# Kernel tuning notes

Hardware: AMD Instinct MI355X
Metric: run time of the kernel (lower is better)

The kernel has to match this reference:

```python
import jax, jax.numpy as jnp
import numpy as np

B, L, K = 4, 2048, 30
NS, NV = 1024, 256   # node hidden (scalar, vector)
ES, EV = 32, 1       # edge hidden (scalar, vector)
CLAMP = 32           # clamp_rel_pos
PE = 16              # num positional embeddings

def _nan_to_num(t):
    return jnp.where(jnp.isfinite(t), t, jnp.zeros((), t.dtype))

def _norm(t, axis=-1, keepdims=False, eps=1e-8):
    return jnp.sqrt(jnp.sum(t * t, axis=axis, keepdims=keepdims) + eps)

def _normalize(t, axis=-1):
    return _nan_to_num(t / _norm(t, axis=axis, keepdims=True))

def _norm_no_nan(t, axis=-1, keepdims=False, eps=1e-8, sqrt=True):
    out = jnp.maximum(jnp.sum(t * t, axis=axis, keepdims=keepdims), eps)
    return jnp.sqrt(out) if sqrt else out

def _rbf(values, v_min, v_max, n_bins=16):
    centers = jnp.linspace(v_min, v_max, n_bins)
    std = (v_max - v_min) / n_bins
    z = (values[..., None] - centers) / std
    return jnp.exp(-z * z)

def _dihedrals(X, eps=1e-7):
    b = X.shape[0]
    Xf = X[:, :, :3].reshape(b, -1, 3)           # [B, 3L, 3]
    U = _normalize(Xf[:, 1:] - Xf[:, :-1])
    u2, u1, u0 = U[:, :-2], U[:, 1:-1], U[:, 2:]
    n2 = _normalize(jnp.cross(u2, u1))
    n1 = _normalize(jnp.cross(u1, u0))
    cosD = jnp.clip(jnp.sum(n2 * n1, -1), -1 + eps, 1 - eps)
    D = jnp.sign(jnp.sum(u2 * n1, -1)) * jnp.arccos(cosD)
    D = jnp.pad(D, ((0, 0), (1, 2))).reshape(b, -1, 3)
    return jnp.concatenate([jnp.cos(D), jnp.sin(D)], -1)   # [B,L,6]

def _orientations(Xca):
    f = jnp.pad(_normalize(Xca[:, 1:] - Xca[:, :-1]), ((0, 0), (0, 1), (0, 0)))
    bk = jnp.pad(_normalize(Xca[:, :-1] - Xca[:, 1:]), ((0, 0), (1, 0), (0, 0)))
    return jnp.concatenate([f[:, :, None], bk[:, :, None]], -2)  # [B,L,2,3]

def _sidechains(X):
    n, origin, c = X[:, :, 0], X[:, :, 1], X[:, :, 2]
    c, n = _normalize(c - origin), _normalize(n - origin)
    bisector = _normalize(c + n)
    perp = _normalize(jnp.cross(c, n))
    return -bisector * float(np.sqrt(1.0 / 3.0)) - perp * float(np.sqrt(2.0 / 3.0))

def _dist(Xca, coord_mask, res_idx, padding_mask, k, order=3):
    n = Xca.shape[1]
    cmf = coord_mask.astype(jnp.float32)
    cm2 = cmf[:, None, :] * cmf[:, :, None]
    rmf = (~padding_mask).astype(jnp.float32)
    rm2 = rmf[:, None, :] * rmf[:, :, None]
    dX = Xca[:, None, :, :] - Xca[:, :, None, :]
    D = cm2 * _norm(dX, axis=-1)
    cov = (jnp.abs(res_idx[:, :, None] - res_idx[:, None, :]) <= order).astype(jnp.float32)
    D_cov = D * (1.0 - cov)
    seqpos = jnp.arange(n)
    Dseq = jnp.abs(seqpos[:, None] - seqpos[None, :]).astype(jnp.float32)
    D_adjust = _nan_to_num(D_cov) + (1.0 - cm2) * (1e8 + Dseq * 1e6) + (1.0 - rm2) * 1e10
    _, E_idx = jax.lax.top_k(-D_adjust, k)                # k smallest
    D_neighbors = jnp.take_along_axis(D, E_idx, axis=-1)  # regather raw D (as in source)
    return D_neighbors, E_idx, D_neighbors < 5e7, D_neighbors < 5e9

def _edge_features(coords, coord_mask, res_idx, padding_mask):
    Xca = coords[:, :, 1]
    E_dist, E_idx, E_cm, E_rm = _dist(Xca, coord_mask, res_idx, padding_mask, K)
    b, n, k = E_idx.shape
    src = jnp.broadcast_to(jnp.arange(n, dtype=E_idx.dtype)[None, :, None], (b, n, k))
    edge_index = jnp.stack([src, E_idx], 0).reshape(2, b, n * k)
    E_dist = E_dist.reshape(b, n * k)
    E_cm = E_cm.reshape(b, n * k)
    E_rm = E_rm.reshape(b, n * k)
    E_cmf = E_cm[..., None].astype(jnp.float32)
    edge_start = jnp.take_along_axis(res_idx, edge_index[0], axis=-1)
    edge_end = jnp.take_along_axis(res_idx, edge_index[1], axis=-1)
    d = jnp.clip(edge_start - edge_end, -CLAMP, CLAMP).astype(jnp.float32)
    freq = jnp.exp(jnp.arange(0, PE, 2, dtype=jnp.float32) * (-np.log(10000.0) / PE))
    ang = d[..., None] * freq
    pos = jnp.concatenate([jnp.cos(ang), jnp.sin(ang)], -1)
    D_rbf = _rbf(E_dist, 0.0, 20.0)
    X_src = jnp.broadcast_to(Xca[:, :, None, :], (b, n, k, 3)).reshape(b, n * k, 3)
    X_dest = jnp.take_along_axis(Xca, edge_index[1][..., None], axis=1)
    cm_src = jnp.broadcast_to(coord_mask[:, :, None], (b, n, k)).reshape(b, n * k)
    cm_dest = jnp.take_along_axis(coord_mask, edge_index[1], axis=1)
    E_vec = X_src - X_dest
    E_mean = jnp.sum(E_vec * E_cmf, 1, keepdims=True) / jnp.sum(E_cmf, 1, keepdims=True)
    E_vec = E_vec * E_cmf + E_mean * (1.0 - E_cmf)
    edge_s = _nan_to_num(jnp.concatenate([D_rbf, pos], -1))
    edge_v = _nan_to_num(_normalize(E_vec)[:, :, None, :])
    edge_s = jnp.concatenate([edge_s,
                              (~cm_src).astype(jnp.float32)[..., None],
                              (~cm_dest).astype(jnp.float32)[..., None]], -1)  # [B,Lk,34]
    invalid = (~E_rm) | (~E_cm)   # remove_edges_without_coords=True
    edge_index = jnp.where(invalid[None], -1, edge_index)
    return edge_s, edge_v, jnp.transpose(edge_index, (1, 0, 2)), invalid

def _gvp(s, v, wh, ws_w, ws_b, wv):
    # v: [..., vi, 3]; activations=(None, None), vector_gate=False
    vh = jnp.einsum('...id,ih->...hd', v, wh)       # [..., h, 3]
    vn = _norm_no_nan(vh, axis=-1)                  # [..., h]
    s_out = jnp.concatenate([s, vn], -1) @ ws_w + ws_b
    v_out = jnp.einsum('...hd,hv->...vd', vh, wv)
    return s_out, v_out

def _gvp_layernorm(s, v, gamma, beta, eps=1e-4):
    mu = jnp.mean(s, -1, keepdims=True)
    var = jnp.mean((s - mu) ** 2, -1, keepdims=True)
    s_out = (s - mu) / jnp.sqrt(var + eps) * gamma + beta
    vn2 = _norm_no_nan(v, axis=-1, keepdims=True, sqrt=False)
    v_out = v / jnp.sqrt(jnp.mean(vn2, axis=-2, keepdims=True))
    return s_out, v_out

def _forward(coords, coord_mask, res_idx, padding_mask, confidence,
             node_wh, node_ws_w, node_ws_b, node_wv, node_ln_g, node_ln_b,
             edge_wh, edge_ws_w, edge_ws_b, edge_wv, edge_ln_g, edge_ln_b,
             conf_w, conf_b):
    node_s = jnp.concatenate([_dihedrals(coords),
                              coord_mask.astype(jnp.float32)[..., None]], -1)  # [B,L,7]
    node_v = jnp.concatenate([_orientations(coords[:, :, 1]),
                              _sidechains(coords)[:, :, None]], -2)            # [B,L,3,3]
    edge_s, edge_v, edge_index, invalid = _edge_features(coords, coord_mask, res_idx, padding_mask)
    # torch.no_grad() over featurization
    node_s, node_v, edge_s, edge_v = map(jax.lax.stop_gradient,
                                         (node_s, node_v, edge_s, edge_v))
    ns, nv = _gvp_layernorm(*_gvp(node_s, node_v, node_wh, node_ws_w, node_ws_b, node_wv),
                            node_ln_g, node_ln_b)
    es, ev = _gvp_layernorm(*_gvp(edge_s, edge_v, edge_wh, edge_ws_w, edge_ws_b, edge_wv),
                            edge_ln_g, edge_ln_b)
    ns = ns + _rbf(confidence, 0.0, 1.0) @ conf_w + conf_b
    b = ns.shape[0]
    ns = ns.reshape(b * L, NS)
    nv = nv.reshape(b * L, NV, 3)
    es = es.reshape(b * L * K, ES)
    ev = ev.reshape(b * L * K, EV, 3)
    # flatten_graph (padded: invalid edges kept with index -1, embeddings zeroed)
    valid = (~invalid).reshape(-1)
    ei = edge_index + (jnp.arange(b, dtype=edge_index.dtype) * L)[:, None, None]
    ei = jnp.transpose(ei, (1, 0, 2)).reshape(2, -1)
    ei = jnp.where(valid[None, :], ei, -1)
    es = jnp.where(valid[:, None], es, 0.0)
    ev = jnp.where(valid[:, None, None], ev, 0.0)
    return ns, nv, es, ev, ei

def setup_inputs():
    key = jax.random.key(0)
    ks = jax.random.split(key, 12)
    def lin(k, fan_in, shape):
        return jax.random.normal(k, shape, jnp.float32) / np.sqrt(fan_in)
    return {
        'coords': jax.random.normal(ks[0], (B, L, 3, 3), jnp.float32),
        'coord_mask': jax.random.randint(ks[1], (B, L), 0, 2) > 0,
        'res_idx': jnp.arange(B * L, dtype=jnp.int32).reshape(B, L),
        'padding_mask': jnp.zeros((B, L), dtype=bool),
        'confidence': jax.random.uniform(ks[2], (B, L), jnp.float32),
        'node_wh': lin(ks[3], 3, (3, NV)),
        'node_ws_w': lin(ks[4], NV + 7, (NV + 7, NS)),
        'node_ws_b': jnp.zeros((NS,), jnp.float32),
        'node_wv': lin(ks[5], NV, (NV, NV)),
        'node_ln_g': jnp.ones((NS,), jnp.float32),
        'node_ln_b': jnp.zeros((NS,), jnp.float32),
        'edge_wh': lin(ks[6], 1, (1, 1)),
        'edge_ws_w': lin(ks[7], 35, (35, ES)),
        'edge_ws_b': jnp.zeros((ES,), jnp.float32),
        'edge_wv': lin(ks[8], 1, (1, 1)),
        'edge_ln_g': jnp.ones((ES,), jnp.float32),
        'edge_ln_b': jnp.zeros((ES,), jnp.float32),
        'conf_w': lin(ks[9], 16, (16, NS)),
        'conf_b': jnp.zeros((NS,), jnp.float32),
    }

def reference(coords, coord_mask, res_idx, padding_mask, confidence,
              node_wh, node_ws_w, node_ws_b, node_wv, node_ln_g, node_ln_b,
              edge_wh, edge_ws_w, edge_ws_b, edge_wv, edge_ln_g, edge_ln_b,
              conf_w, conf_b):
    return _forward(coords, coord_mask, res_idx, padding_mask, confidence,
                    node_wh, node_ws_w, node_ws_b, node_wv, node_ln_g, node_ln_b,
                    edge_wh, edge_ws_w, edge_ws_b, edge_wv, edge_ln_g, edge_ln_b,
                    conf_w, conf_b)
```

## Files before the change

kernel.cpp:

```cpp
#include <hip/hip_runtime.h>
#include <math.h>

constexpr int Bc = 4, Lc = 2048, Kc = 30;
constexpr int Nn = Bc * Lc;
constexpr int NSc = 1024, NVc = 256;
constexpr int NEc = Nn * Kc;
constexpr int SK = 263;

constexpr size_t OUT_NS = 0;
constexpr size_t OUT_NV = (size_t)Nn * NSc;
constexpr size_t OUT_ES = OUT_NV + (size_t)Nn * NVc * 3;
constexpr size_t OUT_EV = OUT_ES + (size_t)NEc * 32;
constexpr size_t OUT_EI = OUT_EV + (size_t)NEc * 3;

constexpr size_t WS_SIN = 0;
constexpr size_t WS_NDV = WS_SIN + (size_t)Nn * SK;
constexpr size_t WS_EIX = WS_NDV + (size_t)Nn * 9;
constexpr size_t WS_EDS = WS_EIX + (size_t)NEc;
constexpr size_t WS_CMF = WS_EDS + (size_t)NEc;

__device__ __forceinline__ void norml3(float& x, float& y, float& z) {
  float ss = x*x + y*y + z*z;
  float inv = 1.0f / sqrtf(ss + 1e-8f);
  x *= inv; y *= inv; z *= inv;
}

__global__ __launch_bounds__(256) void kmask(const unsigned char* __restrict__ cm,
                                             const float* __restrict__ coords,
                                             const int* __restrict__ resid,
                                             const unsigned char* __restrict__ pmask,
                                             float* __restrict__ ws,
                                             float4* __restrict__ pack) {
  __shared__ int flag;
  if (threadIdx.x == 0) flag = 0;
  __syncthreads();
  int any = 0;
  for (int p = threadIdx.x; p < 1024; p += 256)
    if (p & 3) any |= cm[p];
  if (any) atomicOr(&flag, 1);
  __syncthreads();
  bool bytefmt = (flag != 0);
  int n = blockIdx.x * 256 + threadIdx.x;
  unsigned char v = bytefmt ? cm[n] : cm[4*n];
  ws[WS_CMF + n] = v ? 1.f : 0.f;
  int rm = (pmask[n] == 0) ? 1 : 0;
  int w = (resid[n] << 2) | ((v ? 1 : 0) << 1) | rm;
  float4 p;
  p.x = coords[(size_t)n*9 + 3];
  p.y = coords[(size_t)n*9 + 4];
  p.z = coords[(size_t)n*9 + 5];
  p.w = __int_as_float(w);
  pack[n] = p;
}

__global__ __launch_bounds__(256) void kwhwv(const float* __restrict__ wh,
                                             const float* __restrict__ wv,
                                             float4* __restrict__ whwv4,
                                             float4* __restrict__ wht4) {
  __shared__ float r0[256], r1[256], r2[256];
  int tid = threadIdx.x, lane = tid & 63, wid = tid >> 6;
  int vcol = blockIdx.x * 64 + lane;
  float a0 = 0.f, a1 = 0.f, a2 = 0.f;
  #pragma unroll 4
  for (int hh = 0; hh < 64; ++hh) {
    int h = wid * 64 + hh;
    float wvv = wv[(size_t)h * 256 + vcol];
    a0 = fmaf(wh[h],       wvv, a0);
    a1 = fmaf(wh[256 + h], wvv, a1);
    a2 = fmaf(wh[512 + h], wvv, a2);
  }
  r0[tid] = a0; r1[tid] = a1; r2[tid] = a2;
  __syncthreads();
  if (wid == 0) {
    a0 = r0[lane] + r0[lane+64] + r0[lane+128] + r0[lane+192];
    a1 = r1[lane] + r1[lane+64] + r1[lane+128] + r1[lane+192];
    a2 = r2[lane] + r2[lane+64] + r2[lane+128] + r2[lane+192];
    whwv4[vcol] = float4{a0, a1, a2, 0.f};
  } else if (wid == 1) {
    wht4[vcol] = float4{wh[vcol], wh[256 + vcol], wh[512 + vcol], 0.f};
  }
}

__global__ __launch_bounds__(256) void knode_geom(const float* __restrict__ coords,
                                                  float* __restrict__ ws) {
  int n = blockIdx.x * 256 + threadIdx.x;
  if (n >= Nn) return;
  int b = n / Lc, l = n % Lc;
  const float* Xb = coords + (size_t)b * Lc * 9;
  float ax[7][3];
  #pragma unroll
  for (int m = 0; m < 7; ++m) {
    int t = 3*l + m - 2;
    if (t >= 0 && t < 3*Lc) { ax[m][0]=Xb[t*3+0]; ax[m][1]=Xb[t*3+1]; ax[m][2]=Xb[t*3+2]; }
    else { ax[m][0]=0.f; ax[m][1]=0.f; ax[m][2]=0.f; }
  }
  float U[5][3];
  #pragma unroll
  for (int mi = 0; mi < 5; ++mi) {
    int t = 3*l - 1 + mi;
    if (t >= 0 && t <= 3*Lc - 2) {
      float x = ax[mi+2][0]-ax[mi+1][0], y = ax[mi+2][1]-ax[mi+1][1], z = ax[mi+2][2]-ax[mi+1][2];
      norml3(x,y,z);
      U[mi][0]=x; U[mi][1]=y; U[mi][2]=z;
    } else { U[mi][0]=0.f; U[mi][1]=0.f; U[mi][2]=0.f; }
  }
  float cph[3], sph[3];
  #pragma unroll
  for (int a = 0; a < 3; ++a) {
    int t = 3*l + a - 1;
    if (t < 0 || t > 3*Lc - 4) { cph[a] = 1.f; sph[a] = 0.f; continue; }
    const float *u2 = U[a], *u1 = U[a+1], *u0 = U[a+2];
    float n2x = u2[1]*u1[2]-u2[2]*u1[1], n2y = u2[2]*u1[0]-u2[0]*u1[2], n2z = u2[0]*u1[1]-u2[1]*u1[0];
    norml3(n2x,n2y,n2z);
    float n1x = u1[1]*u0[2]-u1[2]*u0[1], n1y = u1[2]*u0[0]-u1[0]*u0[2], n1z = u1[0]*u0[1]-u1[1]*u0[0];
    norml3(n1x,n1y,n1z);
    float cd = n2x*n1x + n2y*n1y + n2z*n1z;
    cd = fminf(fmaxf(cd, -1.f + 1e-7f), 1.f - 1e-7f);
    float dt = u2[0]*n1x + u2[1]*n1y + u2[2]*n1z;
    float sg = (dt > 0.f) ? 1.f : ((dt < 0.f) ? -1.f : 0.f);
    float D = sg * acosf(cd);
    cph[a] = cosf(D); sph[a] = sinf(D);
  }
  float fx=0.f,fy=0.f,fz=0.f, kx=0.f,ky=0.f,kz=0.f;
  if (l < Lc-1) { fx=ax[6][0]-ax[3][0]; fy=ax[6][1]-ax[3][1]; fz=ax[6][2]-ax[3][2]; norml3(fx,fy,fz); }
  if (l > 0)    { kx=ax[0][0]-ax[3][0]; ky=ax[0][1]-ax[3][1]; kz=ax[0][2]-ax[3][2]; norml3(kx,ky,kz); }
  float cx=ax[4][0]-ax[3][0], cy=ax[4][1]-ax[3][1], cz=ax[4][2]-ax[3][2]; norml3(cx,cy,cz);
  float nx=ax[2][0]-ax[3][0], ny=ax[2][1]-ax[3][1], nz=ax[2][2]-ax[3][2]; norml3(nx,ny,nz);
  float bix=cx+nx, biy=cy+ny, biz=cz+nz; norml3(bix,biy,biz);
  float px=cy*nz-cz*ny, py=cz*nx-cx*nz, pz=cx*ny-cy*nx; norml3(px,py,pz);
  const float c1 = 0.57735026f, c2 = 0.81649658f;
  float sx = -bix*c1 - px*c2, sy = -biy*c1 - py*c2, sz = -biz*c1 - pz*c2;

  float cmf = ws[WS_CMF + n];
  float* sr = ws + WS_SIN + (size_t)n * SK;
  sr[0]=cph[0]; sr[1]=cph[1]; sr[2]=cph[2]; sr[3]=sph[0]; sr[4]=sph[1]; sr[5]=sph[2]; sr[6]=cmf;
  float* vr = ws + WS_NDV + (size_t)n * 9;
  vr[0]=fx; vr[1]=fy; vr[2]=fz; vr[3]=kx; vr[4]=ky; vr[5]=kz; vr[6]=sx; vr[7]=sy; vr[8]=sz;
}

__global__ __launch_bounds__(256) void kvnode(const float4* __restrict__ wht4,
                                              const float4* __restrict__ whwv4,
                                              float* __restrict__ ws,
                                              float* __restrict__ out) {
  int tid = threadIdx.x, lane = tid & 63, wid = tid >> 6;
  int n = blockIdx.x * 4 + wid;
  const float* v = ws + WS_NDV + (size_t)n * 9;
  float v00=v[0],v01=v[1],v02=v[2];
  float v10=v[3],v11=v[4],v12=v[5];
  float v20=v[6],v21=v[7],v22=v[8];
  float p = 0.f;
  float vo[4][3];
  #pragma unroll
  for (int m = 0; m < 4; ++m) {
    int h = lane + 64*m;
    float4 wt = wht4[h];
    float vh0 = v00*wt.x + v10*wt.y + v20*wt.z;
    float vh1 = v01*wt.x + v11*wt.y + v21*wt.z;
    float vh2 = v02*wt.x + v12*wt.y + v22*wt.z;
    ws[WS_SIN + (size_t)n*SK + 7 + h] = sqrtf(fmaxf(vh0*vh0 + vh1*vh1 + vh2*vh2, 1e-8f));
    float4 wc = whwv4[h];
    float o0 = v00*wc.x + v10*wc.y + v20*wc.z;
    float o1 = v01*wc.x + v11*wc.y + v21*wc.z;
    float o2 = v02*wc.x + v12*wc.y + v22*wc.z;
    vo[m][0]=o0; vo[m][1]=o1; vo[m][2]=o2;
    p += fmaxf(o0*o0 + o1*o1 + o2*o2, 1e-8f);
  }
  #pragma unroll
  for (int off = 1; off < 64; off <<= 1) p += __shfl_xor(p, off);
  float isd = 1.f / sqrtf(p * (1.f/256.f));
  #pragma unroll
  for (int m = 0; m < 4; ++m) {
    size_t o = OUT_NV + (size_t)n*768 + (size_t)(lane + 64*m)*3;
    out[o+0] = vo[m][0]*isd;
    out[o+1] = vo[m][1]*isd;
    out[o+2] = vo[m][2]*isd;
  }
}

__global__ __launch_bounds__(256) void ktopk(const float4* __restrict__ pack,
                                             float* __restrict__ ws) {
  __shared__ unsigned long long cbuf[4][256];
  int tid = threadIdx.x, lane = tid & 63, wid = tid >> 6;
  int row = blockIdx.x * 4 + wid;
  int b = row >> 11;
  int i = row & (Lc - 1);
  const float4* P = pack + (size_t)b * Lc;
  int* eix = (int*)(ws + WS_EIX);
  unsigned long long lmask_lt = (1ULL << lane) - 1ULL;

  float4 pi = P[i];
  int wi = __float_as_int(pi.w);
  float cmi = ((wi >> 1) & 1) ? 1.f : 0.f;
  float rmi = (wi & 1) ? 1.f : 0.f;
  int ri = wi >> 2;

  unsigned a[32];
  unsigned lmin = 0xFFFFFFFFu;
  #pragma unroll
  for (int m = 0; m < 32; ++m) {
    int j = lane + 64*m;
    float4 pj = P[j];
    int wj = __float_as_int(pj.w);
    float cmj = ((wj >> 1) & 1) ? 1.f : 0.f;
    float rmj = (wj & 1) ? 1.f : 0.f;
    float dx = __fsub_rn(pi.x, pj.x);
    float dy = __fsub_rn(pi.y, pj.y);
    float dz = __fsub_rn(pi.z, pj.z);
    float ss = __fadd_rn(__fadd_rn(__fmul_rn(dx,dx), __fmul_rn(dy,dy)), __fmul_rn(dz,dz));
    float dist = __fsqrt_rn(__fadd_rn(ss, 1e-8f));
    float cm2 = __fmul_rn(cmi, cmj);
    float D = __fmul_rn(cm2, dist);
    int ad = ri - (wj >> 2); ad = ad < 0 ? -ad : ad;
    float covm = (ad <= 3) ? 0.f : 1.f;
    float dseq = (float)(i >= j ? i - j : j - i);
    float t1 = __fmul_rn(__fsub_rn(1.f, cm2), __fadd_rn(1e8f, __fmul_rn(dseq, 1e6f)));
    float rm2 = __fmul_rn(rmi, rmj);
    float t2 = __fmul_rn(__fsub_rn(1.f, rm2), 1e10f);
    float adj = __fadd_rn(__fadd_rn(__fmul_rn(D, covm), t1), t2);
    unsigned u = __float_as_uint(adj);
    a[m] = u;
    lmin = u < lmin ? u : lmin;
  }

  unsigned lo = 0u, hi = 0xFFFFFFFFu;
  while (lo < hi) {
    unsigned mid = lo + ((hi - lo) >> 1);
    unsigned long long bal = __ballot(lmin <= mid);
    if (__popcll(bal) >= Kc) hi = mid; else lo = mid + 1u;
  }
  unsigned Tv = lo;

  unsigned base = 0;
  #pragma unroll
  for (int m = 0; m < 32; ++m) {
    bool pred = (a[m] <= Tv);
    unsigned long long bal = __ballot(pred);
    if (pred) {
      unsigned pos = base + (unsigned)__popcll(bal & lmask_lt);
      if (pos < 256u)
        cbuf[wid][pos] = ((unsigned long long)a[m] << 32) | (unsigned)(lane + 64*m);
    }
    base += (unsigned)__popcll(bal);
  }
  unsigned M = base < 256u ? base : 256u;
  __builtin_amdgcn_wave_barrier();

  for (unsigned idx = (unsigned)lane; idx < M; idx += 64u) {
    unsigned long long k0 = cbuf[wid][idx];
    int rank = 0;
    for (unsigned t = 0; t < M; ++t) rank += (cbuf[wid][t] < k0) ? 1 : 0;
    if (rank < Kc) {
      int j = (int)(k0 & 2047ULL);
      float4 pj = P[j];
      int wj = __float_as_int(pj.w);
      float cmj = ((wj >> 1) & 1) ? 1.f : 0.f;
      float dx = __fsub_rn(pi.x, pj.x);
      float dy = __fsub_rn(pi.y, pj.y);
      float dz = __fsub_rn(pi.z, pj.z);
      float ss2 = __fadd_rn(__fadd_rn(__fmul_rn(dx,dx), __fmul_rn(dy,dy)), __fmul_rn(dz,dz));
      float dist = __fsqrt_rn(__fadd_rn(ss2, 1e-8f));
      float D = __fmul_rn(__fmul_rn(cmi, cmj), dist);
      eix[(size_t)row*Kc + rank] = j;
      ws[WS_EDS + (size_t)row*Kc + rank] = D;
    }
  }
}

__global__ __launch_bounds__(256) void kgemm_s(const float* __restrict__ ws,
                                               const float* __restrict__ wsw,
                                               const float* __restrict__ wsb,
                                               float* __restrict__ out) {
  __shared__ __align__(16) float As[16][132];
  __shared__ __align__(16) float Bs[16][64];
  int tid = threadIdx.x;
  int lb = (int)(blockIdx.x & 7) * 128 + (int)(blockIdx.x >> 3);
  int by = lb >> 4, bx = lb & 15;
  int row0 = by * 128, cn0 = bx * 64;
  int tx = tid & 15, ty = tid >> 4;
  int aka = tid & 15;
  int arw = tid >> 4;
  int bkk = tid >> 4;
  int bc4 = tid & 15;
  const float* Abase = ws + WS_SIN;
  float acc[8][4] = {};
  for (int k0 = 0; k0 < SK; k0 += 16) {
    int ka = k0 + aka;
    bool kaok = (ka < SK);
    #pragma unroll
    for (int i = 0; i < 8; ++i) {
      int r = arw + 16*i;
      As[aka][r] = kaok ? Abase[(size_t)(row0 + r)*SK + ka] : 0.f;
    }
    {
      int kb = k0 + bkk;
      float4 v = (kb < SK) ? *(const float4*)&wsw[(size_t)kb*NSc + cn0 + bc4*4]
                           : float4{0.f,0.f,0.f,0.f};
      *(float4*)&Bs[bkk][bc4*4] = v;
    }
    __syncthreads();
    #pragma unroll 4
    for (int kk = 0; kk < 16; ++kk) {
      float4 a0 = *(const float4*)&As[kk][ty*8 + 0];
      float4 a1 = *(const float4*)&As[kk][ty*8 + 4];
      float4 b4 = *(const float4*)&Bs[kk][tx*4];
      float av[8] = {a0.x,a0.y,a0.z,a0.w, a1.x,a1.y,a1.z,a1.w};
      float bv[4] = {b4.x,b4.y,b4.z,b4.w};
      #pragma unroll
      for (int r = 0; r < 8; ++r)
        #pragma unroll
        for (int c = 0; c < 4; ++c)
          acc[r][c] = fmaf(av[r], bv[c], acc[r][c]);
    }
    __syncthreads();
  }
  float4 bb = *(const float4*)&wsb[cn0 + tx*4];
  #pragma unroll
  for (int r = 0; r < 8; ++r) {
    size_t o = OUT_NS + (size_t)(row0 + ty*8 + r)*NSc + cn0 + tx*4;
    float4 ov = {acc[r][0]+bb.x, acc[r][1]+bb.y, acc[r][2]+bb.z, acc[r][3]+bb.w};
    *(float4*)&out[o] = ov;
  }
}

__global__ __launch_bounds__(256) void kedge(const float* __restrict__ coords,
    const int* __restrict__ resid,
    const float* __restrict__ ewh, const float* __restrict__ eww,
    const float* __restrict__ ewb, const float* __restrict__ ewv,
    const float* __restrict__ elg, const float* __restrict__ elb,
    const float* __restrict__ ws, float* __restrict__ out) {
  __shared__ float w[35*32];
  __shared__ float wb[32], g[32], bb[32];
  int tid = threadIdx.x;
  for (int t = tid; t < 35*32; t += 256) w[t] = eww[t];
  if (tid < 32) { wb[tid] = ewb[tid]; g[tid] = elg[tid]; bb[tid] = elb[tid]; }
  __syncthreads();
  int e = blockIdx.x * 256 + tid;
  if (e >= NEc) return;
  int b = e / (Lc*Kc);
  int rem = e - b*(Lc*Kc);
  int i = rem / Kc;
  int row = b*Lc + i;
  const int* eix = (const int*)(ws + WS_EIX);
  int j = eix[e];
  float Dn = ws[WS_EDS + e];
  bool jok = ((unsigned)j < (unsigned)Lc);
  bool valid = jok && (Dn < 5e7f) && (Dn < 5e9f);
  if (!valid) {
    #pragma unroll
    for (int c = 0; c < 32; ++c) out[OUT_ES + (size_t)e*32 + c] = 0.f;
    out[OUT_EV + (size_t)e*3 + 0] = 0.f;
    out[OUT_EV + (size_t)e*3 + 1] = 0.f;
    out[OUT_EV + (size_t)e*3 + 2] = 0.f;
    out[OUT_EI + e]       = -1.f;
    out[OUT_EI + NEc + e] = -1.f;
    return;
  }
  int dcl = resid[row] - resid[b*Lc + j];
  dcl = dcl < -32 ? -32 : (dcl > 32 ? 32 : dcl);
  float dpos = (float)dcl;
  float s[35];
  #pragma unroll
  for (int m = 0; m < 16; ++m) {
    float c = (20.f/15.f) * (float)m;
    float z = (Dn - c) * 0.8f;
    s[m] = expf(-z*z);
  }
  #pragma unroll
  for (int m = 0; m < 8; ++m) {
    float fr = expf((float)(2*m) * (-0.57564627324851148f));
    float ang = dpos * fr;
    s[16+m] = cosf(ang);
    s[24+m] = sinf(ang);
  }
  float csf = ws[WS_CMF + row];
  float cdf = ws[WS_CMF + b*Lc + j];
  s[32] = 1.f - csf; s[33] = 1.f - cdf;
  const float* Xb = coords + (size_t)b*Lc*9;
  float vx = Xb[i*9+3] - Xb[j*9+3];
  float vy = Xb[i*9+4] - Xb[j*9+4];
  float vz = Xb[i*9+5] - Xb[j*9+5];
  float ss2 = vx*vx + vy*vy + vz*vz;
  float inv = 1.f / sqrtf(ss2 + 1e-8f);
  float e0 = vx*inv, e1 = vy*inv, e2 = vz*inv;
  if (!isfinite(e0)) e0 = 0.f;
  if (!isfinite(e1)) e1 = 0.f;
  if (!isfinite(e2)) e2 = 0.f;
  float wh00 = ewh[0], wv00 = ewv[0];
  float vh0 = e0*wh00, vh1 = e1*wh00, vh2 = e2*wh00;
  s[34] = sqrtf(fmaxf(vh0*vh0 + vh1*vh1 + vh2*vh2, 1e-8f));
  float o[32]; float sm = 0.f;
  #pragma unroll
  for (int c = 0; c < 32; ++c) {
    float a = wb[c];
    #pragma unroll
    for (int q = 0; q < 35; ++q) a = fmaf(s[q], w[q*32 + c], a);
    o[c] = a; sm += a;
  }
  float mu = sm * (1.f/32.f);
  float sq = 0.f;
  #pragma unroll
  for (int c = 0; c < 32; ++c) { float dd = o[c]-mu; sq += dd*dd; }
  float isd = 1.f / sqrtf(sq*(1.f/32.f) + 1e-4f);
  float vo0 = vh0*wv00, vo1 = vh1*wv00, vo2 = vh2*wv00;
  float vn2 = fmaxf(vo0*vo0 + vo1*vo1 + vo2*vo2, 1e-8f);
  float ivn = 1.f / sqrtf(vn2);
  #pragma unroll
  for (int c = 0; c < 32; ++c)
    out[OUT_ES + (size_t)e*32 + c] = (o[c]-mu)*isd*g[c] + bb[c];
  out[OUT_EV + (size_t)e*3 + 0] = vo0*ivn;
  out[OUT_EV + (size_t)e*3 + 1] = vo1*ivn;
  out[OUT_EV + (size_t)e*3 + 2] = vo2*ivn;
  out[OUT_EI + e]       = (float)row;
  out[OUT_EI + NEc + e] = (float)(b*Lc + j);
}

__global__ __launch_bounds__(256) void kln_node(const float* __restrict__ conf,
    const float* __restrict__ cw, const float* __restrict__ cb,
    const float* __restrict__ lg, const float* __restrict__ lb,
    float* __restrict__ out) {
  int n = blockIdx.x, tid = threadIdx.x;
  size_t base = OUT_NS + (size_t)n*NSc;
  float x0 = out[base + tid];
  float x1 = out[base + tid + 256];
  float x2 = out[base + tid + 512];
  float x3 = out[base + tid + 768];
  float sm = x0+x1+x2+x3;
  float sq = x0*x0+x1*x1+x2*x2+x3*x3;
  int lane = tid & 63, wid = tid >> 6;
  #pragma unroll
  for (int off = 32; off > 0; off >>= 1) { sm += __shfl_down(sm, off); sq += __shfl_down(sq, off); }
  __shared__ float rs[4], rq[4];
  if (lane == 0) { rs[wid] = sm; rq[wid] = sq; }
  __syncthreads();
  sm = rs[0]+rs[1]+rs[2]+rs[3];
  sq = rq[0]+rq[1]+rq[2]+rq[3];
  float mu = sm * (1.f/1024.f);
  float var = fmaxf(sq * (1.f/1024.f) - mu*mu, 0.f);
  float isd = 1.f / sqrtf(var + 1e-4f);
  float cf = conf[n];
  float rb[16];
  #pragma unroll
  for (int m = 0; m < 16; ++m) {
    float z = (cf - (float)m*(1.f/15.f)) * 16.f;
    rb[m] = expf(-z*z);
  }
  float xs_[4] = {x0, x1, x2, x3};
  #pragma unroll
  for (int q = 0; q < 4; ++q) {
    int c = tid + q*256;
    float t = cb[c];
    #pragma unroll
    for (int m = 0; m < 16; ++m) t = fmaf(rb[m], cw[m*1024 + c], t);
    out[base + c] = (xs_[q]-mu)*isd*lg[c] + lb[c] + t;
  }
}

extern "C" void kernel_launch(void* const* d_in, const int* in_sizes, int n_in,
                              void* d_out, int out_size, void* d_ws, size_t ws_size,
                              hipStream_t stream) {
  const float* coords         = (const float*)d_in[0];
  const unsigned char* cmask  = (const unsigned char*)d_in[1];
  const int* resid            = (const int*)d_in[2];
  const unsigned char* pmask  = (const unsigned char*)d_in[3];
  const float* conf           = (const float*)d_in[4];
  const float* nwh            = (const float*)d_in[5];
  const float* nww            = (const float*)d_in[6];
  const float* nwb            = (const float*)d_in[7];
  const float* nwv            = (const float*)d_in[8];
  const float* nlg            = (const float*)d_in[9];
  const float* nlb            = (const float*)d_in[10];
  const float* ewh            = (const float*)d_in[11];
  const float* eww            = (const float*)d_in[12];
  const float* ewb            = (const float*)d_in[13];
  const float* ewv            = (const float*)d_in[14];
  const float* elg            = (const float*)d_in[15];
  const float* elb            = (const float*)d_in[16];
  const float* cw             = (const float*)d_in[17];
  const float* cb             = (const float*)d_in[18];
  float* out = (float*)d_out;
  float* ws  = (float*)d_ws;
  float4* whwv4 = (float4*)(out + OUT_ES);
  float4* wht4  = whwv4 + 256;
  float4* pack  = (float4*)(out + OUT_EV);

  kmask<<<Nn/256, 256, 0, stream>>>(cmask, coords, resid, pmask, ws, pack);
  kwhwv<<<4, 256, 0, stream>>>(nwh, nwv, whwv4, wht4);
  knode_geom<<<(Nn+255)/256, 256, 0, stream>>>(coords, ws);
  kvnode<<<Nn/4, 256, 0, stream>>>(wht4, whwv4, ws, out);
  ktopk<<<Nn/4, 256, 0, stream>>>(pack, ws);
  kgemm_s<<<(Nn/128)*(NSc/64), 256, 0, stream>>>(ws, nww, nwb, out);
  kedge<<<NEc/256, 256, 0, stream>>>(coords, resid, ewh, eww, ewb, ewv, elg, elb, ws, out);
  kln_node<<<Nn, 256, 0, stream>>>(conf, cw, cb, nlg, nlb, out);
}
```

Baseline: 298.8 us.

## Merge init kernels, shrink node_geom blocks, double-buffer GEMM K-loop via registers

Merges the mask/pack kernel and the wh·wv precompute into one launch, which removes one kernel launch. Shrinks knode_geom blocks to 64 threads so its 8192 threads spread over more CUs. Rewrites the scalar node GEMM with a K-tile of 32 and register prefetch of the next tile while the current tile is computed, so global-load latency overlaps with FMA work. The larger shared-memory tiles and extra prefetch registers may reduce occupancy.

```diff
diff --git a/kernel.cpp b/kernel.cpp
--- a/kernel.cpp
+++ b/kernel.cpp
@@ -25,65 +25,67 @@
   x *= inv; y *= inv; z *= inv;
 }
 
-__global__ __launch_bounds__(256) void kmask(const unsigned char* __restrict__ cm,
+__global__ __launch_bounds__(256) void kinit(const unsigned char* __restrict__ cm,
                                              const float* __restrict__ coords,
                                              const int* __restrict__ resid,
                                              const unsigned char* __restrict__ pmask,
+                                             const float* __restrict__ wh,
+                                             const float* __restrict__ wv,
                                              float* __restrict__ ws,
-                                             float4* __restrict__ pack) {
-  __shared__ int flag;
-  if (threadIdx.x == 0) flag = 0;
-  __syncthreads();
-  int any = 0;
-  for (int p = threadIdx.x; p < 1024; p += 256)
-    if (p & 3) any |= cm[p];
-  if (any) atomicOr(&flag, 1);
-  __syncthreads();
-  bool bytefmt = (flag != 0);
-  int n = blockIdx.x * 256 + threadIdx.x;
-  unsigned char v = bytefmt ? cm[n] : cm[4*n];
-  ws[WS_CMF + n] = v ? 1.f : 0.f;
-  int rm = (pmask[n] == 0) ? 1 : 0;
-  int w = (resid[n] << 2) | ((v ? 1 : 0) << 1) | rm;
-  float4 p;
-  p.x = coords[(size_t)n*9 + 3];
-  p.y = coords[(size_t)n*9 + 4];
-  p.z = coords[(size_t)n*9 + 5];
-  p.w = __int_as_float(w);
-  pack[n] = p;
-}
-
-__global__ __launch_bounds__(256) void kwhwv(const float* __restrict__ wh,
-                                             const float* __restrict__ wv,
+                                             float4* __restrict__ pack,
                                              float4* __restrict__ whwv4,
                                              float4* __restrict__ wht4) {
   __shared__ float r0[256], r1[256], r2[256];
-  int tid = threadIdx.x, lane = tid & 63, wid = tid >> 6;
-  int vcol = blockIdx.x * 64 + lane;
-  float a0 = 0.f, a1 = 0.f, a2 = 0.f;
-  #pragma unroll 4
-  for (int hh = 0; hh < 64; ++hh) {
-    int h = wid * 64 + hh;
-    float wvv = wv[(size_t)h * 256 + vcol];
-    a0 = fmaf(wh[h],       wvv, a0);
-    a1 = fmaf(wh[256 + h], wvv, a1);
-    a2 = fmaf(wh[512 + h], wvv, a2);
-  }
-  r0[tid] = a0; r1[tid] = a1; r2[tid] = a2;
-  __syncthreads();
-  if (wid == 0) {
-    a0 = r0[lane] + r0[lane+64] + r0[lane+128] + r0[lane+192];
-    a1 = r1[lane] + r1[lane+64] + r1[lane+128] + r1[lane+192];
-    a2 = r2[lane] + r2[lane+64] + r2[lane+128] + r2[lane+192];
-    whwv4[vcol] = float4{a0, a1, a2, 0.f};
-  } else if (wid == 1) {
-    wht4[vcol] = float4{wh[vcol], wh[256 + vcol], wh[512 + vcol], 0.f};
-  }
-}
-
-__global__ __launch_bounds__(256) void knode_geom(const float* __restrict__ coords,
-                                                  float* __restrict__ ws) {
-  int n = blockIdx.x * 256 + threadIdx.x;
+  __shared__ int flag;
+  int tid = threadIdx.x;
+  if (blockIdx.x < 32) {
+    if (tid == 0) flag = 0;
+    __syncthreads();
+    int any = 0;
+    for (int p = tid; p < 1024; p += 256)
+      if (p & 3) any |= cm[p];
+    if (any) atomicOr(&flag, 1);
+    __syncthreads();
+    bool bytefmt = (flag != 0);
+    int n = blockIdx.x * 256 + tid;
+    unsigned char v = bytefmt ? cm[n] : cm[4*n];
+    ws[WS_CMF + n] = v ? 1.f : 0.f;
+    int rm = (pmask[n] == 0) ? 1 : 0;
+    int w = (resid[n] << 2) | ((v ? 1 : 0) << 1) | rm;
+    float4 p;
+    p.x = coords[(size_t)n*9 + 3];
+    p.y = coords[(size_t)n*9 + 4];
+    p.z = coords[(size_t)n*9 + 5];
+    p.w = __int_as_float(w);
+    pack[n] = p;
+  } else {
+    int lane = tid & 63, wid = tid >> 6;
+    int vcol = (int)(blockIdx.x - 32) * 64 + lane;
+    float a0 = 0.f, a1 = 0.f, a2 = 0.f;
+    #pragma unroll 4
+    for (int hh = 0; hh < 64; ++hh) {
+      int h = wid * 64 + hh;
+      float wvv = wv[(size_t)h * 256 + vcol];
+      a0 = fmaf(wh[h],       wvv, a0);
+      a1 = fmaf(wh[256 + h], wvv, a1);
+      a2 = fmaf(wh[512 + h], wvv, a2);
+    }
+    r0[tid] = a0; r1[tid] = a1; r2[tid] = a2;
+    __syncthreads();
+    if (wid == 0) {
+      a0 = r0[lane] + r0[lane+64] + r0[lane+128] + r0[lane+192];
+      a1 = r1[lane] + r1[lane+64] + r1[lane+128] + r1[lane+192];
+      a2 = r2[lane] + r2[lane+64] + r2[lane+128] + r2[lane+192];
+      whwv4[vcol] = float4{a0, a1, a2, 0.f};
+    } else if (wid == 1) {
+      wht4[vcol] = float4{wh[vcol], wh[256 + vcol], wh[512 + vcol], 0.f};
+    }
+  }
+}
+
+__global__ __launch_bounds__(64) void knode_geom(const float* __restrict__ coords,
+                                                 float* __restrict__ ws) {
+  int n = blockIdx.x * 64 + threadIdx.x;
   if (n >= Nn) return;
   int b = n / Lc, l = n % Lc;
   const float* Xb = coords + (size_t)b * Lc * 9;
@@ -270,36 +272,53 @@
                                                const float* __restrict__ wsw,
                                                const float* __restrict__ wsb,
                                                float* __restrict__ out) {
-  __shared__ __align__(16) float As[16][132];
-  __shared__ __align__(16) float Bs[16][64];
+  __shared__ __align__(16) float As[32][132];
+  __shared__ __align__(16) float Bs[32][64];
   int tid = threadIdx.x;
   int lb = (int)(blockIdx.x & 7) * 128 + (int)(blockIdx.x >> 3);
   int by = lb >> 4, bx = lb & 15;
   int row0 = by * 128, cn0 = bx * 64;
   int tx = tid & 15, ty = tid >> 4;
-  int aka = tid & 15;
-  int arw = tid >> 4;
-  int bkk = tid >> 4;
-  int bc4 = tid & 15;
+  int aka = tid & 15, arw = tid >> 4;
+  int bkk = tid >> 4, bc4 = tid & 15;
   const float* Abase = ws + WS_SIN;
+
+  float ar[16];
+  float4 br[2];
+  #pragma unroll
+  for (int h = 0; h < 2; ++h) {
+    int ka = h*16 + aka;
+    #pragma unroll
+    for (int i = 0; i < 8; ++i)
+      ar[h*8+i] = Abase[(size_t)(row0 + arw + 16*i)*SK + ka];
+    br[h] = *(const float4*)&wsw[(size_t)(h*16 + bkk)*NSc + cn0 + bc4*4];
+  }
   float acc[8][4] = {};
-  for (int k0 = 0; k0 < SK; k0 += 16) {
-    int ka = k0 + aka;
-    bool kaok = (ka < SK);
+  for (int k0 = 0; k0 < SK; k0 += 32) {
     #pragma unroll
-    for (int i = 0; i < 8; ++i) {
-      int r = arw + 16*i;
-      As[aka][r] = kaok ? Abase[(size_t)(row0 + r)*SK + ka] : 0.f;
-    }
-    {
-      int kb = k0 + bkk;
-      float4 v = (kb < SK) ? *(const float4*)&wsw[(size_t)kb*NSc + cn0 + bc4*4]
-                           : float4{0.f,0.f,0.f,0.f};
-      *(float4*)&Bs[bkk][bc4*4] = v;
+    for (int h = 0; h < 2; ++h) {
+      #pragma unroll
+      for (int i = 0; i < 8; ++i)
+        As[h*16 + aka][arw + 16*i] = ar[h*8+i];
+      *(float4*)&Bs[h*16 + bkk][bc4*4] = br[h];
     }
     __syncthreads();
+    int kn = k0 + 32;
+    if (kn < SK) {
+      #pragma unroll
+      for (int h = 0; h < 2; ++h) {
+        int ka = kn + h*16 + aka;
+        bool ok = (ka < SK);
+        #pragma unroll
+        for (int i = 0; i < 8; ++i)
+          ar[h*8+i] = ok ? Abase[(size_t)(row0 + arw + 16*i)*SK + ka] : 0.f;
+        int kb = kn + h*16 + bkk;
+        br[h] = (kb < SK) ? *(const float4*)&wsw[(size_t)kb*NSc + cn0 + bc4*4]
+                          : float4{0.f,0.f,0.f,0.f};
+      }
+    }
     #pragma unroll 4
-    for (int kk = 0; kk < 16; ++kk) {
+    for (int kk = 0; kk < 32; ++kk) {
       float4 a0 = *(const float4*)&As[kk][ty*8 + 0];
       float4 a1 = *(const float4*)&As[kk][ty*8 + 4];
       float4 b4 = *(const float4*)&Bs[kk][tx*4];
@@ -483,9 +502,8 @@
   float4* wht4  = whwv4 + 256;
   float4* pack  = (float4*)(out + OUT_EV);
 
-  kmask<<<Nn/256, 256, 0, stream>>>(cmask, coords, resid, pmask, ws, pack);
-  kwhwv<<<4, 256, 0, stream>>>(nwh, nwv, whwv4, wht4);
-  knode_geom<<<(Nn+255)/256, 256, 0, stream>>>(coords, ws);
+  kinit<<<36, 256, 0, stream>>>(cmask, coords, resid, pmask, nwh, nwv, ws, pack, whwv4, wht4);
+  knode_geom<<<Nn/64, 64, 0, stream>>>(coords, ws);
   kvnode<<<Nn/4, 256, 0, stream>>>(wht4, whwv4, ws, out);
   ktopk<<<Nn/4, 256, 0, stream>>>(pack, ws);
   kgemm_s<<<(Nn/128)*(NSc/64), 256, 0, stream>>>(ws, nww, nwb, out);
```

Result: no change. 297.9 us (-0.3%).
